# Optimization experiments

Hardware: AMD Instinct MI355X
Metric: run time of the kernel (lower is better)

## Reference

```python
import jax, jax.numpy as jnp
import numpy as np

NX = 320   # image matrix (nRead)
NC = 8     # coils
NT = 8     # motion states
M = 65536  # non-Cartesian k-space samples per frame
OS = 2     # gridding oversampling factor


def setup_inputs() -> dict:
    key = jax.random.key(0)
    ks = jax.random.split(key, 7)
    kspace_r = jax.random.normal(ks[0], (NC, M), jnp.float32)
    kspace_i = jax.random.normal(ks[1], (NC, M), jnp.float32)
    # k-space trajectory normalized to [-0.5, 0.5)
    traj = jax.random.uniform(ks[2], (M, 2, NT), jnp.float32, -0.5, 0.5)
    csm_r = jax.random.normal(ks[3], (NC, NX, NX), jnp.float32)
    csm_i = jax.random.normal(ks[4], (NC, NX, NX), jnp.float32)
    dcf = jax.random.uniform(ks[5], (M, NT), jnp.float32)
    # motion/flow field in pixels, [NX, NX, 2, NT]
    motions = 3.0 * jax.random.normal(ks[6], (NX, NX, 2, NT), jnp.float32)
    return dict(kspace_r=kspace_r, kspace_i=kspace_i, traj=traj,
                csm_r=csm_r, csm_i=csm_i, dcf=dcf, motions=motions)


def _grid_adjoint(kspace, traj_t, dcf_t, csm):
    """Adjoint NUFFT (gpuNUFFT adj_op): density-compensated bilinear gridding
    onto a 2x oversampled Cartesian grid, inverse FFT, center crop,
    deapodization, and conjugate coil combination."""
    G = OS * NX
    data = (kspace * dcf_t[None, :]).astype(jnp.complex64)  # [NC, M]
    u = (traj_t[:, 0] + 0.5) * G
    v = (traj_t[:, 1] + 0.5) * G
    u0 = jnp.floor(u)
    v0 = jnp.floor(v)
    du = (u - u0).astype(jnp.float32)
    dv = (v - v0).astype(jnp.float32)
    i0 = u0.astype(jnp.int32) % G
    i1 = (i0 + 1) % G
    j0 = v0.astype(jnp.int32) % G
    j1 = (j0 + 1) % G
    grid = jnp.zeros((NC, G, G), jnp.complex64)
    grid = grid.at[:, i0, j0].add(data * ((1.0 - du) * (1.0 - dv)))
    grid = grid.at[:, i1, j0].add(data * (du * (1.0 - dv)))
    grid = grid.at[:, i0, j1].add(data * ((1.0 - du) * dv))
    grid = grid.at[:, i1, j1].add(data * (du * dv))
    im_os = jnp.fft.fftshift(
        jnp.fft.ifft2(jnp.fft.ifftshift(grid, axes=(-2, -1)), axes=(-2, -1)),
        axes=(-2, -1))
    s = (G - NX) // 2
    im = im_os[:, s:s + NX, s:s + NX]  # [NC, NX, NX]
    # deapodization: FT of the triangle (bilinear) gridding kernel is sinc^2
    x = (jnp.arange(NX, dtype=jnp.float32) - NX // 2) / G
    d = jnp.sinc(x) ** 2
    im = im / (d[:, None] * d[None, :])
    # conjugate coil combine with sensitivity maps
    return jnp.sum(jnp.conj(csm) * im, axis=0).astype(jnp.complex64)


def _bilinear_warp(im, flow):
    """apply_sparse_motion: sparse bilinear-interpolation warp of a 2D image
    by a per-pixel displacement field flow[..., 0:2] (in pixels)."""
    Nx, Ny = im.shape
    xs = jnp.arange(Nx, dtype=jnp.float32)[:, None] + flow[..., 0]
    ys = jnp.arange(Ny, dtype=jnp.float32)[None, :] + flow[..., 1]
    xs = jnp.clip(xs, 0.0, Nx - 1.0)
    ys = jnp.clip(ys, 0.0, Ny - 1.0)
    x0 = jnp.floor(xs).astype(jnp.int32)
    y0 = jnp.floor(ys).astype(jnp.int32)
    x1 = jnp.minimum(x0 + 1, Nx - 1)
    y1 = jnp.minimum(y0 + 1, Ny - 1)
    dx = xs - x0.astype(jnp.float32)
    dy = ys - y0.astype(jnp.float32)
    return ((1.0 - dx) * (1.0 - dy) * im[x0, y0]
            + dx * (1.0 - dy) * im[x1, y0]
            + (1.0 - dx) * dy * im[x0, y1]
            + dx * dy * im[x1, y1])


def reference(kspace_r, kspace_i, traj, csm_r, csm_i, dcf, motions):
    kspace = (kspace_r + 1j * kspace_i).astype(jnp.complex64)
    csm = (csm_r + 1j * csm_i).astype(jnp.complex64)

    def frame(traj_t, dcf_t, flow_t):
        im = _grid_adjoint(kspace, traj_t, dcf_t, csm)
        return _bilinear_warp(im, flow_t)

    # vmap over motion states: traj[..., t], dcf[..., t], motions[..., t]
    per_frame = jax.vmap(frame, in_axes=(2, 1, 3))(traj, dcf, motions)  # [NT, NX, NX]
    out = jnp.sum(per_frame, axis=0)  # temporal sum, complex [NX, NX]
    return jnp.stack([out.real, out.imag], axis=-1)  # [NX, NX, 2]
```

## Files before the change

### kernel.cpp

```cpp
#include <hip/hip_runtime.h>
#include <math.h>

#define NXI 320
#define NCI 8
#define NTI 8
#define MI  65536
#define GI  640
#define G2I (GI*GI)
#define NPIX (NXI*NXI)
#define REC_F 20
#define NBINS (NTI*G2I)
#define SCAN_BLKS2 (NBINS/4096)

typedef float v2f __attribute__((ext_vector_type(2)));

__device__ inline v2f cmul(v2f a, v2f b) {
    v2f axx = __builtin_shufflevector(a, a, 0, 0);
    v2f ayy = __builtin_shufflevector(a, a, 1, 1);
    v2f byx = __builtin_shufflevector(b, b, 1, 0);
    v2f r = axx * b;
    v2f t = ayy * byx;
    return r + v2f{-t.x, t.y};
}

template<int H>
__device__ inline float sxf(float x) {
    if constexpr (H == 1) {
        return __int_as_float(__builtin_amdgcn_update_dpp(
            __float_as_int(x), __float_as_int(x), 0xB1, 0xF, 0xF, false));
    } else if constexpr (H == 2) {
        return __int_as_float(__builtin_amdgcn_update_dpp(
            __float_as_int(x), __float_as_int(x), 0x4E, 0xF, 0xF, false));
    } else if constexpr (H == 8) {
        return __int_as_float(__builtin_amdgcn_update_dpp(
            __float_as_int(x), __float_as_int(x), 0x128, 0xF, 0xF, false));
    } else {
        return __shfl_xor(x, H, 64);
    }
}
template<int H>
__device__ inline v2f sxv(v2f v) { return v2f{sxf<H>(v.x), sxf<H>(v.y)}; }

__device__ inline void cell_of(const float* __restrict__ traj, int m, int f,
                               int& i0s, int& j0s, float& du, float& dv)
{
    float tu = traj[(m*2 + 0)*NTI + f];
    float tv = traj[(m*2 + 1)*NTI + f];
    float u = (tu + 0.5f) * (float)GI;
    float v = (tv + 0.5f) * (float)GI;
    float fu = floorf(u), fv = floorf(v);
    du = u - fu; dv = v - fv;
    i0s = (int)fu + GI/2; if (i0s >= GI) i0s -= GI;
    j0s = (int)fv + GI/2; if (j0s >= GI) j0s -= GI;
}

__global__ __launch_bounds__(256) void count_cells(
    const float* __restrict__ traj, int* __restrict__ counts)
{
    int tid = blockIdx.x * 256 + threadIdx.x;
    int f = tid >> 16, m = tid & (MI - 1);
    int i0s, j0s; float du, dv;
    cell_of(traj, m, f, i0s, j0s, du, dv);
    atomicAdd(&counts[f*G2I + i0s*GI + j0s], 1);
}

__device__ inline int wave_incl_scan(int v, int lane) {
    #pragma unroll
    for (int d = 1; d < 64; d <<= 1) {
        int y = __shfl_up(v, d, 64);
        if (lane >= d) v += y;
    }
    return v;
}

__global__ __launch_bounds__(1024) void scanA(const int4* __restrict__ counts4,
                                              int4* __restrict__ binstart4,
                                              int* __restrict__ sums)
{
    __shared__ int wtot[16];
    int tid = threadIdx.x, lane = tid & 63, wv = tid >> 6;
    int i = blockIdx.x * 1024 + tid;
    int4 c = counts4[i];
    int s = c.x + c.y + c.z + c.w;
    int incl = wave_incl_scan(s, lane);
    if (lane == 63) wtot[wv] = incl;
    __syncthreads();
    if (wv == 0 && lane < 16) {
        int t = wtot[lane];
        #pragma unroll
        for (int d = 1; d < 16; d <<= 1) {
            int y = __shfl_up(t, d, 64);
            if (lane >= d) t += y;
        }
        wtot[lane] = t;
    }
    __syncthreads();
    int woff = wv ? wtot[wv - 1] : 0;
    int excl = woff + incl - s;
    int4 b;
    b.x = excl; b.y = excl + c.x; b.z = b.y + c.y; b.w = b.z + c.z;
    binstart4[i] = b;
    if (tid == 1023) sums[blockIdx.x] = woff + incl;
}

__global__ __launch_bounds__(1024) void scanB(int* __restrict__ sums,
                                              int* __restrict__ binstart)
{
    __shared__ int tmp[1024];
    int tid = threadIdx.x;
    int v = (tid < SCAN_BLKS2) ? sums[tid] : 0;
    tmp[tid] = v; __syncthreads();
    for (int d = 1; d < 1024; d <<= 1) {
        int y = (tid >= d) ? tmp[tid - d] : 0;
        __syncthreads();
        tmp[tid] += y;
        __syncthreads();
    }
    int incl = tmp[tid];
    if (tid < SCAN_BLKS2) sums[tid] = incl - v;
    if (tid == SCAN_BLKS2 - 1) {
        sums[SCAN_BLKS2] = incl;
        binstart[NBINS] = 0;
    }
}

__global__ __launch_bounds__(256) void scatter_cells(
    const float* __restrict__ kr, const float* __restrict__ ki,
    const float* __restrict__ traj, const float* __restrict__ dcf,
    int* __restrict__ counts, const int* __restrict__ binstart,
    const int* __restrict__ sums, float* __restrict__ recs)
{
    int tid = blockIdx.x * 256 + threadIdx.x;
    int f = tid >> 16, m = tid & (MI - 1);
    int i0s, j0s; float du, dv;
    cell_of(traj, m, f, i0s, j0s, du, dv);
    float w = dcf[m*NTI + f];
    int bin = f*G2I + i0s*GI + j0s;
    int within = atomicSub(&counts[bin], 1) - 1;
    int slot = binstart[bin] + sums[bin >> 12] + within;
    float4* r = (float4*)(recs + (size_t)slot * REC_F);
    r[0] = make_float4(du, dv, 0.f, 0.f);
    #pragma unroll
    for (int q = 0; q < 4; ++q) {
        int c0 = 2*q;
        r[1+q] = make_float4(kr[c0*MI + m]*w,     ki[c0*MI + m]*w,
                             kr[(c0+1)*MI + m]*w, ki[(c0+1)*MI + m]*w);
    }
}

__device__ inline void dft5p(v2f x0, v2f x1, v2f x2, v2f x3, v2f x4, v2f* X)
{
    const float c1 = 0.309016994f, c2 = -0.809016994f;
    const float s1 = 0.951056516f, s2 =  0.587785252f;
    v2f S1 = x1 + x4, D1 = x1 - x4;
    v2f S2 = x2 + x3, D2 = x2 - x3;
    X[0] = x0 + S1 + S2;
    v2f A = x0 + c1*S1 + c2*S2;
    v2f T = s1*D1 + s2*D2;
    v2f B = x0 + c2*S1 + c1*S2;
    v2f U = s2*D1 - s1*D2;
    v2f iT = v2f{-T.y, T.x};
    v2f iU = v2f{-U.y, U.x};
    X[1] = A + iT;  X[4] = A - iT;
    X[2] = B + iU;  X[3] = B - iU;
}

template<int H, int S>
__device__ inline void bf_stage(v2f* a, int lane)
{
    const float PI = 3.14159265358979f;
    bool low = (lane & H) == 0;
    int kp = (lane << S) & 31;
    float sn, cs;
    __sincosf((2.0f * PI / 64.0f) * (float)kp, &sn, &cs);
    v2f w = low ? v2f{1.f, 0.f} : v2f{cs, sn};
    float sg = low ? 1.f : -1.f;
    v2f sgv = v2f{sg, sg};
    #pragma unroll
    for (int n = 0; n < 10; ++n) {
        v2f p = sxv<H>(a[n]);
        v2f t = sgv * a[n] + p;
        a[n] = cmul(t, w);
    }
}

__device__ inline void fft640_pruned(v2f* a, int lane, v2f* line, int xorm)
{
    const float PI = 3.14159265358979f;
    bf_stage<32, 0>(a, lane);
    bf_stage<16, 1>(a, lane);
    bf_stage< 8, 2>(a, lane);
    bf_stage< 4, 3>(a, lane);
    bf_stage< 2, 4>(a, lane);
    bf_stage< 1, 5>(a, lane);
    int k1 = __brev(lane) >> 26;
    float th2 = (2.0f * PI / 640.0f) * (float)k1;
    float sn, cs;
    __sincosf(th2, &sn, &cs);
    v2f wb = v2f{cs, sn};
    v2f w = wb;
    #pragma unroll
    for (int n = 1; n < 10; ++n) {
        a[n] = cmul(a[n], w);
        w = cmul(w, wb);
    }
    v2f E[5], O[5];
    dft5p(a[0], a[2], a[4], a[6], a[8], E);
    dft5p(a[1], a[3], a[5], a[7], a[9], O);
    const v2f tk1 = { 0.809016994f, 0.587785252f};
    const v2f tk2 = { 0.309016994f, 0.951056516f};
    const v2f tk3 = {-0.309016994f, 0.951056516f};
    const v2f tk4 = {-0.809016994f, 0.587785252f};
    v2f t1 = cmul(tk1, O[1]);
    v2f t2 = cmul(tk2, O[2]);
    v2f t3 = cmul(tk3, O[3]);
    v2f t4 = cmul(tk4, O[4]);
    bool hi = (k1 >= 32);
    line[(160 + k1) ^ xorm] = E[0] + O[0];
    line[(224 + k1) ^ xorm] = E[1] + t1;
    int yx = hi ? (k1 - 32) : (288 + k1);
    v2f zx = hi ? (E[2] - t2) : (E[2] + t2);
    line[yx ^ xorm] = zx;
    line[(32 + k1) ^ xorm] = E[3] - t3;
    line[(96 + k1) ^ xorm] = E[4] - t4;
}

__global__ __launch_bounds__(512, 8) void row_fft(
    const int* __restrict__ binstart, const int* __restrict__ sums,
    const float* __restrict__ recs, v2f* __restrict__ rowout)
{
    __shared__ v2f A[NCI][GI];
    int bid = blockIdx.x;
    int i = bid % GI;
    int f = bid / GI;
    int tid = threadIdx.x;
    int im1 = i ? i - 1 : GI - 1;
    const int base0 = f*G2I + i*GI;
    const int base1 = f*G2I + im1*GI;

    #define GS(b) (binstart[b] + sums[(b) >> 12])

    for (int j = tid; j < GI; j += 512) {
        v2f acc[NCI];
        #pragma unroll
        for (int c = 0; c < NCI; ++c) acc[c] = v2f{0.f, 0.f};
        #pragma unroll
        for (int p = 0; p < 2; ++p) {
            const int base = p ? base1 : base0;
            if (j > 0) {
                int lo = GS(base + j - 1), mid = GS(base + j), hi = GS(base + j + 1);
                for (int s = lo; s < hi; ++s) {
                    const float4* R = (const float4*)(recs + (size_t)s*REC_F);
                    float4 h4 = R[0];
                    float wr = p ? h4.x : (1.f - h4.x);
                    float w  = wr * ((s < mid) ? h4.y : (1.f - h4.y));
                    float4 d0 = R[1], d1 = R[2], d2 = R[3], d3 = R[4];
                    acc[0] += w * v2f{d0.x, d0.y};  acc[1] += w * v2f{d0.z, d0.w};
                    acc[2] += w * v2f{d1.x, d1.y};  acc[3] += w * v2f{d1.z, d1.w};
                    acc[4] += w * v2f{d2.x, d2.y};  acc[5] += w * v2f{d2.z, d2.w};
                    acc[6] += w * v2f{d3.x, d3.y};  acc[7] += w * v2f{d3.z, d3.w};
                }
            } else {
                #pragma unroll
                for (int side = 0; side < 2; ++side) {
                    int b = base + (side ? 0 : (GI - 1));
                    int s0 = GS(b), s1 = GS(b + 1);
                    for (int s = s0; s < s1; ++s) {
                        const float4* R = (const float4*)(recs + (size_t)s*REC_F);
                        float4 h4 = R[0];
                        float wr = p ? h4.x : (1.f - h4.x);
                        float w  = wr * (side ? (1.f - h4.y) : h4.y);
                        float4 d0 = R[1], d1 = R[2], d2 = R[3], d3 = R[4];
                        acc[0] += w * v2f{d0.x, d0.y};  acc[1] += w * v2f{d0.z, d0.w};
                        acc[2] += w * v2f{d1.x, d1.y};  acc[3] += w * v2f{d1.z, d1.w};
                        acc[4] += w * v2f{d2.x, d2.y};  acc[5] += w * v2f{d2.z, d2.w};
                        acc[6] += w * v2f{d3.x, d3.y};  acc[7] += w * v2f{d3.z, d3.w};
                    }
                }
            }
        }
        #pragma unroll
        for (int c = 0; c < NCI; ++c) A[c][j] = acc[c];
    }
    #undef GS
    __syncthreads();

    int wv = tid >> 6, lane = tid & 63;
    v2f a[10];
    #pragma unroll
    for (int n = 0; n < 10; ++n) a[n] = A[wv][10*lane + n];
    fft640_pruned(a, lane, A[wv], 0);
    v2f* dst = rowout + (((size_t)f*NCI + wv)*GI + i)*NXI;
    #pragma unroll
    for (int q = 0; q < 5; ++q) {
        int yc = lane + 64*q;
        dst[yc] = A[wv][yc];
    }
}

__global__ __launch_bounds__(512, 8) void col_fft(
    const v2f* __restrict__ rowout, v2f* __restrict__ colimg)
{
    __shared__ v2f A[8][GI];
    int bid = blockIdx.x;
    int g = bid % 40;
    int c = (bid / 40) % NCI;
    int f = bid / (40*NCI);
    int y0 = g * 8;
    int tid = threadIdx.x;
    const v2f* src = rowout + ((size_t)f*NCI + c)*GI*NXI + y0;
    for (int idx = tid; idx < 8*GI; idx += 512) {
        int l = idx & 7, k = idx >> 3;
        A[l][k ^ (4*(l & 3))] = src[(size_t)k*NXI + l];
    }
    __syncthreads();
    int wv = tid >> 6, lane = tid & 63;
    int xm = 4 * (wv & 3);
    v2f a[10];
    #pragma unroll
    for (int n = 0; n < 10; ++n) a[n] = A[wv][(10*lane + n) ^ xm];
    fft640_pruned(a, lane, A[wv], xm);
    __syncthreads();
    v2f* dst = colimg + ((size_t)f*NCI + c)*NPIX + y0;
    for (int idx = tid; idx < 8*NXI; idx += 512) {
        int l = idx & 7, xx = idx >> 3;
        dst[(size_t)xx*NXI + l] = A[l][xx ^ (4*(l & 3))];
    }
}

__global__ __launch_bounds__(256) void combine_kernel(
    const float2* __restrict__ colimg, const float* __restrict__ csr,
    const float* __restrict__ csi, float2* __restrict__ img)
{
    int f = blockIdx.y;
    int pix = blockIdx.x * 256 + threadIdx.x;
    int x = pix / NXI, y = pix - x*NXI;
    const float PI = 3.14159265358979f;
    float tx = (x - 160) * (1.0f/GI);
    float ty = (y - 160) * (1.0f/GI);
    float dx = 1.0f, dy = 1.0f;
    if (x != 160) { float s = __sinf(PI*tx) / (PI*tx); dx = s*s; }
    if (y != 160) { float s = __sinf(PI*ty) / (PI*ty); dy = s*s; }
    float scale = 1.0f / ((float)G2I * dx * dy);
    float accr = 0.f, acci = 0.f;
    #pragma unroll
    for (int c = 0; c < NCI; ++c) {
        float2 g = colimg[((size_t)f*NCI + c)*NPIX + pix];
        float cr = csr[c*NPIX + pix];
        float ci = csi[c*NPIX + pix];
        accr += cr*g.x + ci*g.y;
        acci += cr*g.y - ci*g.x;
    }
    img[(size_t)f*NPIX + pix] = make_float2(accr*scale, acci*scale);
}

__global__ __launch_bounds__(256) void warp_sum(
    const float2* __restrict__ img, const float* __restrict__ motions,
    float* __restrict__ out)
{
    int pix = blockIdx.x * 256 + threadIdx.x;
    int x = pix / NXI, y = pix - x*NXI;
    float accr = 0.f, acci = 0.f;
    #pragma unroll
    for (int f = 0; f < NTI; ++f) {
        float fx = motions[(size_t)(pix*2 + 0)*NTI + f];
        float fy = motions[(size_t)(pix*2 + 1)*NTI + f];
        float xs = fminf(fmaxf((float)x + fx, 0.0f), (float)(NXI-1));
        float ys = fminf(fmaxf((float)y + fy, 0.0f), (float)(NXI-1));
        int x0 = (int)floorf(xs);
        int y0 = (int)floorf(ys);
        int x1 = min(x0+1, NXI-1);
        int y1 = min(y0+1, NXI-1);
        float dx = xs - (float)x0;
        float dy = ys - (float)y0;
        const float2* im = img + (size_t)f*NPIX;
        float2 v00 = im[x0*NXI + y0];
        float2 v10 = im[x1*NXI + y0];
        float2 v01 = im[x0*NXI + y1];
        float2 v11 = im[x1*NXI + y1];
        float w00 = (1.f-dx)*(1.f-dy), w10 = dx*(1.f-dy);
        float w01 = (1.f-dx)*dy,       w11 = dx*dy;
        accr += w00*v00.x + w10*v10.x + w01*v01.x + w11*v11.x;
        acci += w00*v00.y + w10*v10.y + w01*v01.y + w11*v11.y;
    }
    out[pix*2+0] = accr;
    out[pix*2+1] = acci;
}

extern "C" void kernel_launch(void* const* d_in, const int* in_sizes, int n_in,
                              void* d_out, int out_size, void* d_ws, size_t ws_size,
                              hipStream_t stream)
{
    const float* kr   = (const float*)d_in[0];
    const float* ki   = (const float*)d_in[1];
    const float* traj = (const float*)d_in[2];
    const float* csr  = (const float*)d_in[3];
    const float* csi  = (const float*)d_in[4];
    const float* dcf  = (const float*)d_in[5];
    const float* mot  = (const float*)d_in[6];
    float* out = (float*)d_out;

    char* ws = (char*)d_ws;
    float*  recs     = (float*)ws;
    ws += (size_t)NTI * MI * REC_F * sizeof(float);
    v2f*    rowout   = (v2f*)ws;
    ws += (size_t)NTI * NCI * GI * NXI * sizeof(float2);
    float2* colimg   = (float2*)ws;
    ws += (size_t)NTI * NCI * NPIX * sizeof(float2);
    float2* img      = (float2*)ws;
    ws += (size_t)NTI * NPIX * sizeof(float2);
    int*    counts   = (int*)ws;  ws += (size_t)NBINS * sizeof(int);
    int*    binstart = (int*)ws;  ws += ((size_t)NBINS + 16) * sizeof(int);
    int*    sums     = (int*)ws;  ws += 16384;

    hipMemsetAsync(counts, 0, (size_t)NBINS * sizeof(int), stream);
    count_cells  <<<NTI*MI/256, 256, 0, stream>>>(traj, counts);
    scanA        <<<SCAN_BLKS2, 1024, 0, stream>>>((const int4*)counts,
                                                   (int4*)binstart, sums);
    scanB        <<<1,          1024, 0, stream>>>(sums, binstart);
    scatter_cells<<<NTI*MI/256, 256, 0, stream>>>(kr, ki, traj, dcf, counts,
                                                  binstart, sums, recs);
    row_fft      <<<NTI*GI,     512, 0, stream>>>(binstart, sums, recs, rowout);
    col_fft      <<<NTI*NCI*40, 512, 0, stream>>>(rowout, (v2f*)colimg);
    combine_kernel<<<dim3(NPIX/256, NTI), 256, 0, stream>>>(colimg, csr, csi, img);
    warp_sum     <<<NPIX/256,   256, 0, stream>>>(img, mot, out);
}
```

Measured before the change: 288.2 us.

## Fuse column FFT with coil combine via atomics and move deapodization into warp

The column FFT kernel now multiplies each result by the conjugate coil sensitivity and atomically accumulates into the per-frame image, removing the separate combine kernel and the full per-coil image round trip through memory. Deapodization and normalization become a separable per-row/per-column factor table applied at the warp's gather points. Cell records now also store 1-du and 1-dv so the gridding loop skips two subtractions. In exchange the image needs a memset, 8-way float atomic contention per pixel, and a nondeterministic summation order.

```diff
diff --git a/kernel.cpp b/kernel.cpp
--- a/kernel.cpp
+++ b/kernel.cpp
@@ -139,7 +139,7 @@
     int within = atomicSub(&counts[bin], 1) - 1;
     int slot = binstart[bin] + sums[bin >> 12] + within;
     float4* r = (float4*)(recs + (size_t)slot * REC_F);
-    r[0] = make_float4(du, dv, 0.f, 0.f);
+    r[0] = make_float4(du, 1.f - du, dv, 1.f - dv);
     #pragma unroll
     for (int q = 0; q < 4; ++q) {
         int c0 = 2*q;
@@ -252,8 +252,8 @@
                 for (int s = lo; s < hi; ++s) {
                     const float4* R = (const float4*)(recs + (size_t)s*REC_F);
                     float4 h4 = R[0];
-                    float wr = p ? h4.x : (1.f - h4.x);
-                    float w  = wr * ((s < mid) ? h4.y : (1.f - h4.y));
+                    float wr = p ? h4.x : h4.y;
+                    float w  = wr * ((s < mid) ? h4.z : h4.w);
                     float4 d0 = R[1], d1 = R[2], d2 = R[3], d3 = R[4];
                     acc[0] += w * v2f{d0.x, d0.y};  acc[1] += w * v2f{d0.z, d0.w};
                     acc[2] += w * v2f{d1.x, d1.y};  acc[3] += w * v2f{d1.z, d1.w};
@@ -268,8 +268,8 @@
                     for (int s = s0; s < s1; ++s) {
                         const float4* R = (const float4*)(recs + (size_t)s*REC_F);
                         float4 h4 = R[0];
-                        float wr = p ? h4.x : (1.f - h4.x);
-                        float w  = wr * (side ? (1.f - h4.y) : h4.y);
+                        float wr = p ? h4.x : h4.y;
+                        float w  = wr * (side ? h4.w : h4.z);
                         float4 d0 = R[1], d1 = R[2], d2 = R[3], d3 = R[4];
                         acc[0] += w * v2f{d0.x, d0.y};  acc[1] += w * v2f{d0.z, d0.w};
                         acc[2] += w * v2f{d1.x, d1.y};  acc[3] += w * v2f{d1.z, d1.w};
@@ -298,8 +298,9 @@
     }
 }
 
-__global__ __launch_bounds__(512, 8) void col_fft(
-    const v2f* __restrict__ rowout, v2f* __restrict__ colimg)
+__global__ __launch_bounds__(512, 8) void col_fft_combine(
+    const v2f* __restrict__ rowout, const float* __restrict__ csr,
+    const float* __restrict__ csi, float* __restrict__ img)
 {
     __shared__ v2f A[8][GI];
     int bid = blockIdx.x;
@@ -321,42 +322,31 @@
     for (int n = 0; n < 10; ++n) a[n] = A[wv][(10*lane + n) ^ xm];
     fft640_pruned(a, lane, A[wv], xm);
     __syncthreads();
-    v2f* dst = colimg + ((size_t)f*NCI + c)*NPIX + y0;
+    float* imgf = img + (size_t)f * NPIX * 2;
     for (int idx = tid; idx < 8*NXI; idx += 512) {
         int l = idx & 7, xx = idx >> 3;
-        dst[(size_t)xx*NXI + l] = A[l][xx ^ (4*(l & 3))];
-    }
-}
-
-__global__ __launch_bounds__(256) void combine_kernel(
-    const float2* __restrict__ colimg, const float* __restrict__ csr,
-    const float* __restrict__ csi, float2* __restrict__ img)
-{
-    int f = blockIdx.y;
-    int pix = blockIdx.x * 256 + threadIdx.x;
-    int x = pix / NXI, y = pix - x*NXI;
-    const float PI = 3.14159265358979f;
-    float tx = (x - 160) * (1.0f/GI);
-    float ty = (y - 160) * (1.0f/GI);
-    float dx = 1.0f, dy = 1.0f;
-    if (x != 160) { float s = __sinf(PI*tx) / (PI*tx); dx = s*s; }
-    if (y != 160) { float s = __sinf(PI*ty) / (PI*ty); dy = s*s; }
-    float scale = 1.0f / ((float)G2I * dx * dy);
-    float accr = 0.f, acci = 0.f;
-    #pragma unroll
-    for (int c = 0; c < NCI; ++c) {
-        float2 g = colimg[((size_t)f*NCI + c)*NPIX + pix];
+        v2f gv = A[l][xx ^ (4*(l & 3))];
+        int pix = xx*NXI + y0 + l;
         float cr = csr[c*NPIX + pix];
         float ci = csi[c*NPIX + pix];
-        accr += cr*g.x + ci*g.y;
-        acci += cr*g.y - ci*g.x;
-    }
-    img[(size_t)f*NPIX + pix] = make_float2(accr*scale, acci*scale);
+        atomicAdd(&imgf[2*pix + 0], cr*gv.x + ci*gv.y);
+        atomicAdd(&imgf[2*pix + 1], cr*gv.y - ci*gv.x);
+    }
+}
+
+__global__ __launch_bounds__(320) void deapod_init(float* __restrict__ dinv)
+{
+    int x = threadIdx.x;
+    const float PI = 3.14159265358979f;
+    float t = (x - 160) * (1.0f/GI);
+    float d = 1.0f;
+    if (x != 160) { float s = __sinf(PI*t) / (PI*t); d = s*s; }
+    dinv[x] = (1.0f/GI) / d;
 }
 
 __global__ __launch_bounds__(256) void warp_sum(
     const float2* __restrict__ img, const float* __restrict__ motions,
-    float* __restrict__ out)
+    const float* __restrict__ dinv, float* __restrict__ out)
 {
     int pix = blockIdx.x * 256 + threadIdx.x;
     int x = pix / NXI, y = pix - x*NXI;
@@ -373,13 +363,15 @@
         int y1 = min(y0+1, NXI-1);
         float dx = xs - (float)x0;
         float dy = ys - (float)y0;
+        float ax0 = dinv[x0], ax1 = dinv[x1];
+        float ay0 = dinv[y0], ay1 = dinv[y1];
         const float2* im = img + (size_t)f*NPIX;
         float2 v00 = im[x0*NXI + y0];
         float2 v10 = im[x1*NXI + y0];
         float2 v01 = im[x0*NXI + y1];
         float2 v11 = im[x1*NXI + y1];
-        float w00 = (1.f-dx)*(1.f-dy), w10 = dx*(1.f-dy);
-        float w01 = (1.f-dx)*dy,       w11 = dx*dy;
+        float w00 = (1.f-dx)*(1.f-dy)*ax0*ay0, w10 = dx*(1.f-dy)*ax1*ay0;
+        float w01 = (1.f-dx)*dy*ax0*ay1,       w11 = dx*dy*ax1*ay1;
         accr += w00*v00.x + w10*v10.x + w01*v01.x + w11*v11.x;
         acci += w00*v00.y + w10*v10.y + w01*v01.y + w11*v11.y;
     }
@@ -405,15 +397,16 @@
     ws += (size_t)NTI * MI * REC_F * sizeof(float);
     v2f*    rowout   = (v2f*)ws;
     ws += (size_t)NTI * NCI * GI * NXI * sizeof(float2);
-    float2* colimg   = (float2*)ws;
-    ws += (size_t)NTI * NCI * NPIX * sizeof(float2);
     float2* img      = (float2*)ws;
     ws += (size_t)NTI * NPIX * sizeof(float2);
     int*    counts   = (int*)ws;  ws += (size_t)NBINS * sizeof(int);
     int*    binstart = (int*)ws;  ws += ((size_t)NBINS + 16) * sizeof(int);
     int*    sums     = (int*)ws;  ws += 16384;
+    float*  dinv     = (float*)ws; ws += 512 * sizeof(float);
 
     hipMemsetAsync(counts, 0, (size_t)NBINS * sizeof(int), stream);
+    hipMemsetAsync(img, 0, (size_t)NTI * NPIX * sizeof(float2), stream);
+    deapod_init  <<<1, 320, 0, stream>>>(dinv);
     count_cells  <<<NTI*MI/256, 256, 0, stream>>>(traj, counts);
     scanA        <<<SCAN_BLKS2, 1024, 0, stream>>>((const int4*)counts,
                                                    (int4*)binstart, sums);
@@ -421,7 +414,6 @@
     scatter_cells<<<NTI*MI/256, 256, 0, stream>>>(kr, ki, traj, dcf, counts,
                                                   binstart, sums, recs);
     row_fft      <<<NTI*GI,     512, 0, stream>>>(binstart, sums, recs, rowout);
-    col_fft      <<<NTI*NCI*40, 512, 0, stream>>>(rowout, (v2f*)colimg);
-    combine_kernel<<<dim3(NPIX/256, NTI), 256, 0, stream>>>(colimg, csr, csi, img);
-    warp_sum     <<<NPIX/256,   256, 0, stream>>>(img, mot, out);
-}
+    col_fft_combine<<<NTI*NCI*40, 512, 0, stream>>>(rowout, csr, csi, (float*)img);
+    warp_sum     <<<NPIX/256,   256, 0, stream>>>(img, mot, dinv, out);
+}
```

Result: slower. 339.0 us (+17.6%).

## Parallelize row gridding over samples with LDS atomics instead of per-column gather

Applied to the files above, without the earlier changes.

Row gridding now has each thread take one sample record from the two contributing grid rows and scatter its weighted values with shared-memory atomics. Previously each thread owned an output column and gathered from neighbouring bins, which caused load imbalance and read each record twice. The column index is now stored in the record header so the scatter knows where to write. This adds an LDS zeroing pass and many float atomics, which may contend when several samples share a column.

```diff
diff --git a/kernel.cpp b/kernel.cpp
--- a/kernel.cpp
+++ b/kernel.cpp
@@ -139,7 +139,7 @@
     int within = atomicSub(&counts[bin], 1) - 1;
     int slot = binstart[bin] + sums[bin >> 12] + within;
     float4* r = (float4*)(recs + (size_t)slot * REC_F);
-    r[0] = make_float4(du, dv, 0.f, 0.f);
+    r[0] = make_float4(du, dv, (float)j0s, 0.f);
     #pragma unroll
     for (int q = 0; q < 4; ++q) {
         int c0 = 2*q;
@@ -235,54 +235,43 @@
     int f = bid / GI;
     int tid = threadIdx.x;
     int im1 = i ? i - 1 : GI - 1;
-    const int base0 = f*G2I + i*GI;
-    const int base1 = f*G2I + im1*GI;
 
     #define GS(b) (binstart[b] + sums[(b) >> 12])
-
-    for (int j = tid; j < GI; j += 512) {
-        v2f acc[NCI];
-        #pragma unroll
-        for (int c = 0; c < NCI; ++c) acc[c] = v2f{0.f, 0.f};
-        #pragma unroll
-        for (int p = 0; p < 2; ++p) {
-            const int base = p ? base1 : base0;
-            if (j > 0) {
-                int lo = GS(base + j - 1), mid = GS(base + j), hi = GS(base + j + 1);
-                for (int s = lo; s < hi; ++s) {
-                    const float4* R = (const float4*)(recs + (size_t)s*REC_F);
-                    float4 h4 = R[0];
-                    float wr = p ? h4.x : (1.f - h4.x);
-                    float w  = wr * ((s < mid) ? h4.y : (1.f - h4.y));
-                    float4 d0 = R[1], d1 = R[2], d2 = R[3], d3 = R[4];
-                    acc[0] += w * v2f{d0.x, d0.y};  acc[1] += w * v2f{d0.z, d0.w};
-                    acc[2] += w * v2f{d1.x, d1.y};  acc[3] += w * v2f{d1.z, d1.w};
-                    acc[4] += w * v2f{d2.x, d2.y};  acc[5] += w * v2f{d2.z, d2.w};
-                    acc[6] += w * v2f{d3.x, d3.y};  acc[7] += w * v2f{d3.z, d3.w};
-                }
-            } else {
-                #pragma unroll
-                for (int side = 0; side < 2; ++side) {
-                    int b = base + (side ? 0 : (GI - 1));
-                    int s0 = GS(b), s1 = GS(b + 1);
-                    for (int s = s0; s < s1; ++s) {
-                        const float4* R = (const float4*)(recs + (size_t)s*REC_F);
-                        float4 h4 = R[0];
-                        float wr = p ? h4.x : (1.f - h4.x);
-                        float w  = wr * (side ? (1.f - h4.y) : h4.y);
-                        float4 d0 = R[1], d1 = R[2], d2 = R[3], d3 = R[4];
-                        acc[0] += w * v2f{d0.x, d0.y};  acc[1] += w * v2f{d0.z, d0.w};
-                        acc[2] += w * v2f{d1.x, d1.y};  acc[3] += w * v2f{d1.z, d1.w};
-                        acc[4] += w * v2f{d2.x, d2.y};  acc[5] += w * v2f{d2.z, d2.w};
-                        acc[6] += w * v2f{d3.x, d3.y};  acc[7] += w * v2f{d3.z, d3.w};
-                    }
-                }
+    const int rowA = f*G2I + i*GI;
+    const int rowB = f*G2I + im1*GI;
+    int a0 = GS(rowA), a1 = GS(rowA + GI);
+    int b0 = GS(rowB), b1 = GS(rowB + GI);
+    #undef GS
+
+    for (int idx = tid; idx < NCI*GI; idx += 512)
+        ((v2f*)A)[idx] = v2f{0.f, 0.f};
+    __syncthreads();
+
+    float* Af = (float*)A;
+    #pragma unroll
+    for (int p = 0; p < 2; ++p) {
+        int lo = p ? b0 : a0;
+        int hi = p ? b1 : a1;
+        for (int s = lo + tid; s < hi; s += 512) {
+            const float4* R = (const float4*)(recs + (size_t)s*REC_F);
+            float4 h = R[0];
+            int j  = (int)h.z;
+            int j1 = (j + 1 == GI) ? 0 : j + 1;
+            float wu = p ? h.x : (1.f - h.x);
+            float w0 = wu * (1.f - h.y);
+            float w1 = wu * h.y;
+            float4 d0 = R[1], d1 = R[2], d2 = R[3], d3 = R[4];
+            float re[8] = {d0.x, d0.z, d1.x, d1.z, d2.x, d2.z, d3.x, d3.z};
+            float im[8] = {d0.y, d0.w, d1.y, d1.w, d2.y, d2.w, d3.y, d3.w};
+            #pragma unroll
+            for (int c = 0; c < NCI; ++c) {
+                atomicAdd(&Af[(c*GI + j )*2 + 0], w0*re[c]);
+                atomicAdd(&Af[(c*GI + j )*2 + 1], w0*im[c]);
+                atomicAdd(&Af[(c*GI + j1)*2 + 0], w1*re[c]);
+                atomicAdd(&Af[(c*GI + j1)*2 + 1], w1*im[c]);
             }
         }
-        #pragma unroll
-        for (int c = 0; c < NCI; ++c) A[c][j] = acc[c];
-    }
-    #undef GS
+    }
     __syncthreads();
 
     int wv = tid >> 6, lane = tid & 63;
```

New measurement: 433.0 us. 50.2% more time.
